# Performance work log

Hardware: AMD Instinct MI355X
Metric: run time of the kernel (lower is better)

Reference implementation:

```python
import jax, jax.numpy as jnp
import numpy as np

D = 1024      # embedding_dim
H = 16        # n_heads
HD = D // H   # head_dim
EPS = 1e-05


def layernorm(x, scale, bias):
    # torch.var default is unbiased (ddof=1) in the original module
    mean = jnp.mean(x, axis=-1, keepdims=True)
    var = jnp.var(x, axis=-1, keepdims=True, ddof=1)
    return scale * (x - mean) / jnp.sqrt(var + EPS) + bias


def gelu(x):
    return 0.5 * x * (1 + jnp.tanh(0.79788456 * (x + 0.044715 * x ** 3)))


def setup_inputs() -> dict:
    key = jax.random.key(0)
    ks = jax.random.split(key, 12)
    s = 0.02
    return {
        "x": jax.random.normal(ks[0], (2, 2048, D), dtype=jnp.float32),
        "Wq": jax.random.normal(ks[1], (D, D), dtype=jnp.float32) * s,
        "Wk": jax.random.normal(ks[2], (D, D), dtype=jnp.float32) * s,
        "Wv": jax.random.normal(ks[3], (D, D), dtype=jnp.float32) * s,
        "Wo": jax.random.normal(ks[4], (D, D), dtype=jnp.float32) * s,
        "bo": jnp.zeros((D,), dtype=jnp.float32),
        "W1": jax.random.normal(ks[5], (D, 4 * D), dtype=jnp.float32) * s,
        "b1": jnp.zeros((4 * D,), dtype=jnp.float32),
        "W2": jax.random.normal(ks[6], (4 * D, D), dtype=jnp.float32) * s,
        "b2": jnp.zeros((D,), dtype=jnp.float32),
        "ln1_scale": jnp.ones((D,), dtype=jnp.float32),
        "ln1_bias": jnp.zeros((D,), dtype=jnp.float32),
        "ln2_scale": jnp.ones((D,), dtype=jnp.float32),
        "ln2_bias": jnp.zeros((D,), dtype=jnp.float32),
    }


def reference(x, Wq, Wk, Wv, Wo, bo, W1, b1, W2, b2,
              ln1_scale, ln1_bias, ln2_scale, ln2_bias):
    B, S, _ = x.shape
    # --- attention sub-block (pre-LN) ---
    h = layernorm(x, ln1_scale, ln1_bias)
    q = (h @ Wq).reshape(B, S, H, HD).transpose(0, 2, 1, 3)  # [B,H,S,HD]
    k = (h @ Wk).reshape(B, S, H, HD).transpose(0, 2, 1, 3)
    v = (h @ Wv).reshape(B, S, H, HD).transpose(0, 2, 1, 3)
    scores = jnp.einsum("bhqd,bhkd->bhqk", q, k)             # [B,H,S,S]
    causal = jnp.tril(jnp.ones((S, S), dtype=bool))
    scores = jnp.where(causal, scores, -jnp.inf)
    attn = jax.nn.softmax(scores / jnp.sqrt(jnp.float32(HD)), axis=-1)
    ctx = jnp.einsum("bhqk,bhkd->bhqd", attn, v)
    ctx = ctx.transpose(0, 2, 1, 3).reshape(B, S, H * HD)
    x = x + (ctx @ Wo + bo)
    # --- FFN sub-block (pre-LN) ---
    h = layernorm(x, ln2_scale, ln2_bias)
    x = x + (gelu(h @ W1 + b1) @ W2 + b2)
    return x
```

## Files before the change

### kernel.cpp

```cpp
#include <hip/hip_runtime.h>
#include <hip/hip_bf16.h>
#include <cstdint>

#define D_DIM 1024
#define S_DIM 2048
#define B_DIM 2
#define NROWS 4096
#define H_DIM 16
#define LOG2E 1.4426950408889634f
#define QSCALE (0.125f * LOG2E)

typedef __bf16 bf16x8 __attribute__((ext_vector_type(8)));
typedef float f32x4 __attribute__((ext_vector_type(4)));
typedef unsigned short u16x8 __attribute__((ext_vector_type(8)));

#define MFMA16(a, b, c) __builtin_amdgcn_mfma_f32_16x16x32_bf16(a, b, c, 0, 0, 0)
#define SBAR __builtin_amdgcn_sched_barrier(0)
#define WBAR __builtin_amdgcn_s_barrier()
#define LGKM0 { asm volatile("s_waitcnt lgkmcnt(0)" ::: "memory"); SBAR; }
#define VM6 { asm volatile("s_waitcnt vmcnt(6)" ::: "memory"); SBAR; }
#define VM0 { asm volatile("s_waitcnt vmcnt(0)" ::: "memory"); SBAR; }

__device__ __forceinline__ void async_cp16(const void* g, void* lds) {
  __builtin_amdgcn_global_load_lds(
      (const __attribute__((address_space(1))) void*)(uintptr_t)g,
      (__attribute__((address_space(3))) void*)(uint32_t)(uintptr_t)lds, 16, 0, 0);
}

__device__ __forceinline__ unsigned short f2bf(float f) {
  __hip_bfloat16 h = __float2bfloat16(f);
  return __builtin_bit_cast(unsigned short, h);
}

__device__ __forceinline__ float bf2f(unsigned short u) {
  return __builtin_bit_cast(float, (unsigned int)u << 16);
}

__device__ __forceinline__ float gelu_fast(float v) {
  float u = v * v;
  float w = v * fmaf(u, 0.044715f, 1.f);
  float e = exp2f(w * -2.3022161f);
  return v * __builtin_amdgcn_rcpf(1.f + e);
}

struct TcArgs {
  const float* src[6];
  __hip_bfloat16* dst[6];
  int K[6];
  int N[6];
  int start[6];
};

__global__ __launch_bounds__(256) void transpose_cast6_kernel(TcArgs a) {
  __shared__ float tile[32][33];
  int bid = blockIdx.x, mi = 0;
#pragma unroll
  for (int i = 1; i < 6; i++)
    if (bid >= a.start[i]) mi = i;
  const float* W = a.src[mi];
  __hip_bfloat16* Wt = a.dst[mi];
  int K = a.K[mi], N = a.N[mi];
  int rel = bid - a.start[mi];
  int tilesx = N >> 5;
  int shift = (N == 4096) ? 7 : 5;
  int n0 = (rel & (tilesx - 1)) * 32, k0 = (rel >> shift) * 32;
  int tx = threadIdx.x, ty = threadIdx.y;
#pragma unroll
  for (int i = 0; i < 32; i += 8)
    tile[ty + i][tx] = W[(size_t)(k0 + ty + i) * N + n0 + tx];
  __syncthreads();
#pragma unroll
  for (int i = 0; i < 32; i += 8)
    Wt[(size_t)(n0 + ty + i) * K + k0 + tx] = __float2bfloat16(tile[tx][ty + i]);
}

__global__ __launch_bounds__(256) void ln_kernel(
    const float* __restrict__ x, const float* __restrict__ sc,
    const float* __restrict__ bi, __hip_bfloat16* __restrict__ out) {
  int row = blockIdx.x, t = threadIdx.x;
  float4 v = ((const float4*)(x + (size_t)row * D_DIM))[t];
  float s = v.x + v.y + v.z + v.w;
  float ss = v.x * v.x + v.y * v.y + v.z * v.z + v.w * v.w;
#pragma unroll
  for (int off = 32; off > 0; off >>= 1) {
    s += __shfl_xor(s, off);
    ss += __shfl_xor(ss, off);
  }
  __shared__ float red[8];
  int wid = t >> 6;
  if ((t & 63) == 0) { red[wid] = s; red[4 + wid] = ss; }
  __syncthreads();
  s = red[0] + red[1] + red[2] + red[3];
  ss = red[4] + red[5] + red[6] + red[7];
  float mean = s * (1.f / 1024.f);
  float var = (ss - 1024.f * mean * mean) * (1.f / 1023.f);
  float inv = rsqrtf(var + 1e-5f);
  float4 scv = ((const float4*)sc)[t];
  float4 biv = ((const float4*)bi)[t];
  ushort4 o;
  o.x = f2bf(scv.x * (v.x - mean) * inv + biv.x);
  o.y = f2bf(scv.y * (v.y - mean) * inv + biv.y);
  o.z = f2bf(scv.z * (v.z - mean) * inv + biv.z);
  o.w = f2bf(scv.w * (v.w - mean) * inv + biv.w);
  ((ushort4*)(out + (size_t)row * D_DIM))[t] = o;
}

template <int EPI>
__global__ __launch_bounds__(512) void gemm256_kernel(
    const __hip_bfloat16* __restrict__ A, const __hip_bfloat16* __restrict__ Bt,
    void* __restrict__ Cout, const float* __restrict__ bias,
    __hip_bfloat16* __restrict__ qb, __hip_bfloat16* __restrict__ kb,
    unsigned short* __restrict__ vt, int strideA, int strideB) {
  __shared__ char lds[131072];
  const int t = threadIdx.x;
  const int lane = t & 63, wid = t >> 6;
  const int ql = lane & 15, g = lane >> 4;
  const int wr = wid >> 2, wc = wid & 3;
  const int m0 = blockIdx.x * 256, n0 = blockIdx.y * 256;
  const int koff = blockIdx.z * 1024;
  const int sw = (ql & 7) << 4;

  const int srow = t >> 3;
  const int scol = ((t & 7) << 4) ^ ((srow & 7) << 4);
  const __hip_bfloat16* aBase = A + (size_t)(m0 + srow) * strideA + koff + (scol >> 1);
  const __hip_bfloat16* bBase = Bt + (size_t)(n0 + srow) * strideB + koff + (scol >> 1);
  const uint32_t ldsT = (uint32_t)(t * 16);

  auto stgA = [&](int kt, int half) {
    char* dst = lds + ((kt & 1) * 2 + half) * 16384 + ldsT;
    const __hip_bfloat16* src = aBase + (size_t)(half * 128) * strideA + kt * 64;
    async_cp16(src, dst);
    async_cp16(src + (size_t)64 * strideA, dst + 8192);
  };
  auto stgB = [&](int kt, int half) {
    char* dst = lds + 65536 + ((kt & 1) * 2 + half) * 16384 + ldsT;
    const __hip_bfloat16* src = bBase + (size_t)(half * 128) * strideB + kt * 64;
    async_cp16(src, dst);
    async_cp16(src + (size_t)64 * strideB, dst + 8192);
  };

  bf16x8 aR[4][2], bR[2][2][2];
  f32x4 acc[8][4] = {};

  auto ldA = [&](int slot, int mh) {
    const char* base = lds + (slot * 2 + wr) * 16384;
#pragma unroll
    for (int mi = 0; mi < 4; mi++)
#pragma unroll
      for (int kk = 0; kk < 2; kk++)
        aR[mi][kk] = *(const bf16x8*)(base + (mh * 64 + mi * 16 + ql) * 128 +
                                      ((kk * 64 + g * 16) ^ sw));
  };
  auto ldB = [&](int slot, int nh) {
    const char* base = lds + 65536 + (slot * 2 + (wc >> 1)) * 16384;
#pragma unroll
    for (int ni = 0; ni < 2; ni++)
#pragma unroll
      for (int kk = 0; kk < 2; kk++)
        bR[nh][ni][kk] = *(const bf16x8*)(base + ((wc & 1) * 64 + nh * 32 + ni * 16 + ql) * 128 +
                                          ((kk * 64 + g * 16) ^ sw));
  };
  auto mma = [&](int mh, int nh) {
    __builtin_amdgcn_s_setprio(1);
#pragma unroll
    for (int mi = 0; mi < 4; mi++)
#pragma unroll
      for (int ni = 0; ni < 2; ni++) {
        f32x4 c = acc[mh * 4 + mi][nh * 2 + ni];
        c = MFMA16(aR[mi][0], bR[nh][ni][0], c);
        c = MFMA16(aR[mi][1], bR[nh][ni][1], c);
        acc[mh * 4 + mi][nh * 2 + ni] = c;
      }
    __builtin_amdgcn_s_setprio(0);
  };

  stgB(0, 0); stgA(0, 0); stgB(0, 1); stgA(0, 1);
  stgB(1, 0); stgB(1, 1); stgA(1, 0);
  VM6; WBAR;

#pragma unroll 1
  for (int i = 0; i < 7; i++) {
    const int k2 = 2 * i;
    ldA(0, 0); ldB(0, 0); stgA(k2 + 1, 1); SBAR; WBAR; LGKM0; mma(0, 0); WBAR;
    ldB(0, 1); stgB(k2 + 2, 0); SBAR; WBAR; LGKM0; mma(0, 1); WBAR;
    ldA(0, 1); stgB(k2 + 2, 1); SBAR; WBAR; LGKM0; mma(1, 1); WBAR;
    stgA(k2 + 2, 0); SBAR; WBAR; LGKM0; mma(1, 0); VM6; WBAR;
    ldA(1, 0); ldB(1, 0); stgA(k2 + 2, 1); SBAR; WBAR; LGKM0; mma(0, 0); WBAR;
    ldB(1, 1); stgB(k2 + 3, 0); SBAR; WBAR; LGKM0; mma(0, 1); WBAR;
    ldA(1, 1); stgB(k2 + 3, 1); SBAR; WBAR; LGKM0; mma(1, 1); WBAR;
    stgA(k2 + 3, 0); SBAR; WBAR; LGKM0; mma(1, 0); VM6; WBAR;
  }
  ldA(0, 0); ldB(0, 0); stgA(15, 1); SBAR; WBAR; LGKM0; mma(0, 0); WBAR;
  ldB(0, 1); SBAR; WBAR; LGKM0; mma(0, 1); WBAR;
  ldA(0, 1); SBAR; WBAR; LGKM0; mma(1, 1); WBAR;
  SBAR; WBAR; LGKM0; mma(1, 0); VM0; WBAR;
  ldA(1, 0); ldB(1, 0); SBAR; WBAR; LGKM0; mma(0, 0); WBAR;
  ldB(1, 1); SBAR; WBAR; LGKM0; mma(0, 1); WBAR;
  ldA(1, 1); SBAR; WBAR; LGKM0; mma(1, 1); WBAR;
  mma(1, 0);

  const int rb = m0 + wr * 128 + (g << 2);
  const int cb = wc * 64 + ql;
  if (EPI == 0) {
    const int seg = n0 >> 10;
    if (seg < 2) {
      __hip_bfloat16* Ob = seg == 0 ? qb : kb;
      const float sc = seg == 0 ? QSCALE : 1.f;
#pragma unroll
      for (int mb = 0; mb < 8; mb++)
#pragma unroll
        for (int nb = 0; nb < 4; nb++) {
          int col = (n0 & 1023) + cb + nb * 16;
#pragma unroll
          for (int rr = 0; rr < 4; rr++)
            Ob[(size_t)(rb + mb * 16 + rr) * 1024 + col] =
                __float2bfloat16(acc[mb][nb][rr] * sc);
        }
    } else {
#pragma unroll
      for (int mb = 0; mb < 8; mb++)
#pragma unroll
        for (int nb = 0; nb < 4; nb++) {
          int csub = (n0 & 1023) + cb + nb * 16;
          int h = csub >> 6, dh = csub & 63;
          int row0 = rb + mb * 16;
          int bb = row0 >> 11, s0 = row0 & 2047;
          ushort4 pk;
          pk.x = f2bf(acc[mb][nb][0]);
          pk.y = f2bf(acc[mb][nb][1]);
          pk.z = f2bf(acc[mb][nb][2]);
          pk.w = f2bf(acc[mb][nb][3]);
          *(ushort4*)(vt + (((size_t)(bb * 16 + h) * 64 + dh) << 11) + s0) = pk;
        }
    }
  } else if (EPI == 1) {
#pragma unroll
    for (int mb = 0; mb < 8; mb++)
#pragma unroll
      for (int nb = 0; nb < 4; nb++) {
        int col = n0 + cb + nb * 16;
        float bv = bias[col];
#pragma unroll
        for (int rr = 0; rr < 4; rr++)
          ((__hip_bfloat16*)Cout)[(size_t)(rb + mb * 16 + rr) * 4096 + col] =
              __float2bfloat16(gelu_fast(acc[mb][nb][rr] + bv));
      }
  } else {
    unsigned short* Cp = (unsigned short*)Cout + (size_t)blockIdx.z * NROWS * 1024;
#pragma unroll
    for (int mb = 0; mb < 8; mb++)
#pragma unroll
      for (int nb = 0; nb < 4; nb++) {
        int col = n0 + cb + nb * 16;
#pragma unroll
        for (int rr = 0; rr < 4; rr++)
          Cp[(size_t)(rb + mb * 16 + rr) * 1024 + col] = f2bf(acc[mb][nb][rr]);
      }
  }
}

template <int BN, int EPI>
__global__ __launch_bounds__(256) void gemm_bt_kernel(
    const __hip_bfloat16* __restrict__ A, const __hip_bfloat16* __restrict__ Bt,
    void* __restrict__ Cout, const float* __restrict__ bias,
    const float* __restrict__ resid, int M, int N, int K, int kchunk) {
  constexpr int NBF = BN / 32;
  __shared__ __hip_bfloat16 As[2][128 * 32];
  __shared__ __hip_bfloat16 Bs[2][BN * 32];
  const int t = threadIdx.x;
  const int lane = t & 63, wid = t >> 6;
  const int ql = lane & 15, g = lane >> 4;
  const int m0 = blockIdx.x * 128, n0 = blockIdx.y * BN;
  const int kz = blockIdx.z;
  const int wm = (wid >> 1) * 64, wn = (wid & 1) * (BN / 2);
  f32x4 acc[4][NBF] = {};
  const int sr = t >> 2, sc8 = (t & 3) * 8;
  const __hip_bfloat16* ag = A + (size_t)(m0 + sr) * K + sc8 + (size_t)kz * kchunk;
  const __hip_bfloat16* bg = Bt + (size_t)(n0 + sr) * K + sc8 + (size_t)kz * kchunk;

  auto stage = [&](int buf, int k0) {
    async_cp16(ag + k0, (char*)&As[buf][0] + wid * 1024);
    async_cp16(ag + (size_t)64 * K + k0, (char*)&As[buf][0] + 4096 + wid * 1024);
    async_cp16(bg + k0, (char*)&Bs[buf][0] + wid * 1024);
    if constexpr (BN == 128)
      async_cp16(bg + (size_t)64 * K + k0, (char*)&Bs[buf][0] + 4096 + wid * 1024);
  };
  auto compute = [&](int buf) {
    bf16x8 af[4], bfr[NBF];
#pragma unroll
    for (int mb = 0; mb < 4; mb++)
      af[mb] = *(const bf16x8*)(&As[buf][(wm + mb * 16 + ql) * 32 + g * 8]);
#pragma unroll
    for (int nb = 0; nb < NBF; nb++)
      bfr[nb] = *(const bf16x8*)(&Bs[buf][(wn + nb * 16 + ql) * 32 + g * 8]);
#pragma unroll
    for (int mb = 0; mb < 4; mb++)
#pragma unroll
      for (int nb = 0; nb < NBF; nb++)
        acc[mb][nb] = MFMA16(af[mb], bfr[nb], acc[mb][nb]);
  };

  stage(0, 0);
  __syncthreads();
  const int nsteps = kchunk >> 5;
  int cur = 0;
  for (int s = 0; s < nsteps - 1; ++s) {
    stage(cur ^ 1, (s + 1) * 32);
    compute(cur);
    __syncthreads();
    cur ^= 1;
  }
  compute(cur);

  const int rb = m0 + wm + (g << 2);
  const int cb = n0 + wn + ql;
#pragma unroll
  for (int mb = 0; mb < 4; mb++) {
#pragma unroll
    for (int nb = 0; nb < NBF; nb++) {
      int col = cb + nb * 16;
#pragma unroll
      for (int r = 0; r < 4; r++) {
        int row = rb + mb * 16 + r;
        float v = acc[mb][nb][r];
        if (EPI == 1) {
          ((float*)Cout)[(size_t)row * N + col] =
              v + bias[col] + resid[(size_t)row * N + col];
        }
      }
    }
  }
}

__global__ __launch_bounds__(256) void ffn2_reduce_kernel(
    const unsigned short* __restrict__ parts, const float* __restrict__ bias,
    const float* __restrict__ resid, float* __restrict__ out) {
  const size_t i = ((size_t)blockIdx.x * 256 + threadIdx.x) * 8;
  const int col = (int)(i & 1023);
  float a[8];
  float4 r0 = *(const float4*)(resid + i);
  float4 r1 = *(const float4*)(resid + i + 4);
  float4 b0 = *(const float4*)(bias + col);
  float4 b1 = *(const float4*)(bias + col + 4);
  a[0] = r0.x + b0.x; a[1] = r0.y + b0.y; a[2] = r0.z + b0.z; a[3] = r0.w + b0.w;
  a[4] = r1.x + b1.x; a[5] = r1.y + b1.y; a[6] = r1.z + b1.z; a[7] = r1.w + b1.w;
#pragma unroll
  for (int c = 0; c < 4; c++) {
    u16x8 p = *(const u16x8*)(parts + (size_t)c * ((size_t)NROWS * 1024) + i);
#pragma unroll
    for (int j = 0; j < 8; j++) a[j] += bf2f(p[j]);
  }
  float4 o0 = {a[0], a[1], a[2], a[3]};
  float4 o1 = {a[4], a[5], a[6], a[7]};
  *(float4*)(out + i) = o0;
  *(float4*)(out + i + 4) = o1;
}

__global__ __launch_bounds__(256) void attn_kernel(
    const __hip_bfloat16* __restrict__ Q, const __hip_bfloat16* __restrict__ Kb,
    const __hip_bfloat16* __restrict__ Vt, __hip_bfloat16* __restrict__ ctx) {
  __shared__ unsigned short Ks[2][64 * 64];
  __shared__ unsigned short Vs[2][64 * 64];
  __shared__ alignas(16) unsigned short Ps[4][16 * 64];
  const int t = threadIdx.x;
  const int lane = t & 63, wid = t >> 6;
  const int ql = lane & 15, g = lane >> 4;
  const int bid = blockIdx.x;
  const int r4 = bid >> 8, k8 = (bid >> 5) & 7, bh = bid & 31;
  const int qt = (r4 == 0) ? 31 - k8 : (r4 == 1) ? 16 + k8 : (r4 == 2) ? 15 - k8 : k8;
  const int b = bh >> 4, hh = bh & 15;
  const int wq0 = qt * 64 + wid * 16;
  const __hip_bfloat16* qp = Q + (size_t)b * S_DIM * D_DIM + hh * 64;
  const __hip_bfloat16* kp = Kb + (size_t)b * S_DIM * D_DIM + hh * 64;
  const __hip_bfloat16* vp = Vt + (size_t)bh * 64 * S_DIM;
  const int kvend = qt * 64 + 64;
  const int swz = (ql & 7) << 4;
  const f32x4 z4 = {0.f, 0.f, 0.f, 0.f};

  auto stageKV = [&](int buf, int kv0) {
    const int sub = lane >> 3, c = lane & 7;
#pragma unroll
    for (int i = 0; i < 2; i++) {
      const int row = wid * 16 + i * 8 + sub;
      const int cs = (c ^ (row & 7)) * 8;
      async_cp16(kp + (size_t)(kv0 + row) * D_DIM + cs,
                 (char*)&Ks[buf][0] + (wid * 16 + i * 8) * 128);
      async_cp16(vp + (size_t)row * S_DIM + kv0 + cs,
                 (char*)&Vs[buf][0] + (wid * 16 + i * 8) * 128);
    }
  };

  bf16x8 qf[2];
#pragma unroll
  for (int hf = 0; hf < 2; hf++)
    qf[hf] = *(const bf16x8*)(qp + (size_t)(wq0 + ql) * D_DIM + hf * 32 + g * 8);

  float m = -3.0e38f, lsum = 0.f;
  f32x4 acc[4] = {};
  unsigned short* Pw = Ps[wid];

  stageKV(0, 0);
  __syncthreads();
  int cur = 0;
  for (int kv0 = 0; kv0 < kvend; kv0 += 64) {
    if (kv0 + 64 < kvend) stageKV(cur ^ 1, kv0 + 64);

    if (kv0 <= wq0 + 15) {
      const char* Kt = (const char*)&Ks[cur][0];
      f32x4 st[4];
#pragma unroll
      for (int ks = 0; ks < 4; ks++) {
        bf16x8 k0 = *(const bf16x8*)(Kt + (ks * 16 + ql) * 128 + ((g * 16) ^ swz));
        bf16x8 k1 = *(const bf16x8*)(Kt + (ks * 16 + ql) * 128 + (((4 + g) * 16) ^ swz));
        st[ks] = MFMA16(k1, qf[1], MFMA16(k0, qf[0], z4));
      }
      if (kv0 + 63 > wq0) {
#pragma unroll
        for (int ks = 0; ks < 4; ks++)
#pragma unroll
          for (int r = 0; r < 4; r++)
            if (kv0 + ks * 16 + 4 * g + r > wq0 + ql) st[ks][r] = -3.0e38f;
      }
      float tm = -3.0e38f;
#pragma unroll
      for (int ks = 0; ks < 4; ks++)
#pragma unroll
        for (int r = 0; r < 4; r++) tm = fmaxf(tm, st[ks][r]);
      tm = fmaxf(tm, __shfl_xor(tm, 16));
      tm = fmaxf(tm, __shfl_xor(tm, 32));
      if (!__all(tm <= m + 8.f)) {
        const float mn = fmaxf(m, tm);
        const float alpha = exp2f(m - mn);
        lsum *= alpha;
#pragma unroll
        for (int db = 0; db < 4; db++) acc[db] *= alpha;
        m = mn;
      }
      float psum = 0.f;
#pragma unroll
      for (int ks = 0; ks < 4; ks++) {
        float p0 = exp2f(st[ks][0] - m), p1 = exp2f(st[ks][1] - m);
        float p2 = exp2f(st[ks][2] - m), p3 = exp2f(st[ks][3] - m);
        psum += (p0 + p1) + (p2 + p3);
        ushort4 pk;
        pk.x = f2bf(p0); pk.y = f2bf(p1); pk.z = f2bf(p2); pk.w = f2bf(p3);
        *(ushort4*)((char*)Pw + ql * 128 + ((ks * 32 + 8 * g) ^ swz)) = pk;
      }
      psum += __shfl_xor(psum, 16);
      psum += __shfl_xor(psum, 32);
      lsum += psum;

      const char* Vtl = (const char*)&Vs[cur][0];
#pragma unroll
      for (int ksl = 0; ksl < 2; ksl++) {
        bf16x8 pb = *(const bf16x8*)((const char*)Pw + ql * 128 + ((ksl * 64 + 16 * g) ^ swz));
#pragma unroll
        for (int db = 0; db < 4; db++) {
          bf16x8 va = *(const bf16x8*)(Vtl + (db * 16 + ql) * 128 + (((ksl * 4 + g) * 16) ^ swz));
          acc[db] = MFMA16(va, pb, acc[db]);
        }
      }
    }
    __syncthreads();
    cur ^= 1;
  }

  const float inv = 1.f / lsum;
  unsigned short* cp = (unsigned short*)ctx + (size_t)(b * S_DIM + wq0 + ql) * D_DIM + hh * 64;
#pragma unroll
  for (int db = 0; db < 4; db++)
#pragma unroll
    for (int i = 0; i < 2; i++) {
      unsigned int lo = f2bf(acc[db][2 * i] * inv);
      unsigned int hi = f2bf(acc[db][2 * i + 1] * inv);
      *(unsigned int*)(cp + db * 16 + 4 * g + 2 * i) = lo | (hi << 16);
    }
}

extern "C" void kernel_launch(void* const* d_in, const int* in_sizes, int n_in,
                              void* d_out, int out_size, void* d_ws, size_t ws_size,
                              hipStream_t stream) {
  const float* x = (const float*)d_in[0];
  const float* Wq = (const float*)d_in[1];
  const float* Wk = (const float*)d_in[2];
  const float* Wv = (const float*)d_in[3];
  const float* Wo = (const float*)d_in[4];
  const float* bo = (const float*)d_in[5];
  const float* W1 = (const float*)d_in[6];
  const float* b1 = (const float*)d_in[7];
  const float* W2 = (const float*)d_in[8];
  const float* b2 = (const float*)d_in[9];
  const float* ln1s = (const float*)d_in[10];
  const float* ln1b = (const float*)d_in[11];
  const float* ln2s = (const float*)d_in[12];
  const float* ln2b = (const float*)d_in[13];
  float* out = (float*)d_out;

  char* p = (char*)d_ws;
  auto take = [&](size_t n) { char* r = p; p += (n + 255) & ~(size_t)255; return r; };
  __hip_bfloat16* Wqt = (__hip_bfloat16*)take((size_t)1024 * 1024 * 2);
  __hip_bfloat16* Wkt = (__hip_bfloat16*)take((size_t)1024 * 1024 * 2);
  __hip_bfloat16* Wvt = (__hip_bfloat16*)take((size_t)1024 * 1024 * 2);
  __hip_bfloat16* Wot = (__hip_bfloat16*)take((size_t)1024 * 1024 * 2);
  __hip_bfloat16* W1t = (__hip_bfloat16*)take((size_t)4096 * 1024 * 2);
  __hip_bfloat16* W2t = (__hip_bfloat16*)take((size_t)4096 * 1024 * 2);
  __hip_bfloat16* hbuf = (__hip_bfloat16*)take((size_t)NROWS * 1024 * 2);
  __hip_bfloat16* qbuf = (__hip_bfloat16*)take((size_t)NROWS * 1024 * 2);
  __hip_bfloat16* kbuf = (__hip_bfloat16*)take((size_t)NROWS * 1024 * 2);
  __hip_bfloat16* vtbuf = (__hip_bfloat16*)take((size_t)NROWS * 1024 * 2);
  __hip_bfloat16* ctxbuf = (__hip_bfloat16*)take((size_t)NROWS * 1024 * 2);
  float* x1buf = (float*)take((size_t)NROWS * 1024 * 4);
  __hip_bfloat16* h2buf = (__hip_bfloat16*)take((size_t)NROWS * 1024 * 2);
  __hip_bfloat16* gbuf = (__hip_bfloat16*)take((size_t)NROWS * 4096 * 2);
  unsigned short* parts = (unsigned short*)hbuf;

  TcArgs ta;
  ta.src[0] = Wq;  ta.dst[0] = Wqt;  ta.K[0] = 1024; ta.N[0] = 1024; ta.start[0] = 0;
  ta.src[1] = Wk;  ta.dst[1] = Wkt;  ta.K[1] = 1024; ta.N[1] = 1024; ta.start[1] = 1024;
  ta.src[2] = Wv;  ta.dst[2] = Wvt;  ta.K[2] = 1024; ta.N[2] = 1024; ta.start[2] = 2048;
  ta.src[3] = Wo;  ta.dst[3] = Wot;  ta.K[3] = 1024; ta.N[3] = 1024; ta.start[3] = 3072;
  ta.src[4] = W1;  ta.dst[4] = W1t;  ta.K[4] = 1024; ta.N[4] = 4096; ta.start[4] = 4096;
  ta.src[5] = W2;  ta.dst[5] = W2t;  ta.K[5] = 4096; ta.N[5] = 1024; ta.start[5] = 8192;
  transpose_cast6_kernel<<<12288, dim3(32, 8), 0, stream>>>(ta);

  ln_kernel<<<NROWS, 256, 0, stream>>>(x, ln1s, ln1b, hbuf);

  gemm256_kernel<0><<<dim3(16, 12), 512, 0, stream>>>(
      hbuf, Wqt, nullptr, nullptr, qbuf, kbuf, (unsigned short*)vtbuf, 1024, 1024);

  attn_kernel<<<1024, 256, 0, stream>>>(qbuf, kbuf, vtbuf, ctxbuf);

  gemm_bt_kernel<64, 1><<<dim3(32, 16, 1), 256, 0, stream>>>(
      ctxbuf, Wot, x1buf, bo, x, NROWS, 1024, 1024, 1024);

  ln_kernel<<<NROWS, 256, 0, stream>>>(x1buf, ln2s, ln2b, h2buf);

  gemm256_kernel<1><<<dim3(16, 16), 512, 0, stream>>>(
      h2buf, W1t, gbuf, b1, nullptr, nullptr, nullptr, 1024, 1024);

  gemm256_kernel<2><<<dim3(16, 4, 4), 512, 0, stream>>>(
      gbuf, W2t, parts, nullptr, nullptr, nullptr, nullptr, 4096, 4096);

  ffn2_reduce_kernel<<<2048, 256, 0, stream>>>(parts, b2, x1buf, out);
}
```

Baseline: 205.8 us.

## Restructure 256x256 GEMM pipeline with half-tile waits and interleaved warp tile mapping

Changes the warp-to-tile mapping so each warp's A rows and B columns come from both staged LDS halves (interleaved 64-row/32-col slices) instead of one half. The main loop is rescheduled to wait for individual staged halves with fine-grained vmcnt counts. It also drops the explicit lgkmcnt(0) waits and full sched barriers, using a partial sched_barrier mask that lets the compiler place LDS waits. The epilogue is rewritten to match the new accumulator layout. The goal is to overlap global-to-LDS copies with MFMA more tightly and cut barrier stalls, at the risk of subtle ordering bugs in the vmcnt accounting.

```diff
diff --git a/kernel.cpp b/kernel.cpp
--- a/kernel.cpp
+++ b/kernel.cpp
@@ -15,11 +15,9 @@
 typedef unsigned short u16x8 __attribute__((ext_vector_type(8)));
 
 #define MFMA16(a, b, c) __builtin_amdgcn_mfma_f32_16x16x32_bf16(a, b, c, 0, 0, 0)
-#define SBAR __builtin_amdgcn_sched_barrier(0)
+#define SBM __builtin_amdgcn_sched_barrier(0x0F)
 #define WBAR __builtin_amdgcn_s_barrier()
-#define LGKM0 { asm volatile("s_waitcnt lgkmcnt(0)" ::: "memory"); SBAR; }
-#define VM6 { asm volatile("s_waitcnt vmcnt(6)" ::: "memory"); SBAR; }
-#define VM0 { asm volatile("s_waitcnt vmcnt(0)" ::: "memory"); SBAR; }
+#define VMW(n) asm volatile("s_waitcnt vmcnt(" #n ")" ::: "memory")
 
 __device__ __forceinline__ void async_cp16(const void* g, void* lds) {
   __builtin_amdgcn_global_load_lds(
@@ -126,39 +124,37 @@
   const __hip_bfloat16* bBase = Bt + (size_t)(n0 + srow) * strideB + koff + (scol >> 1);
   const uint32_t ldsT = (uint32_t)(t * 16);
 
-  auto stgA = [&](int kt, int half) {
-    char* dst = lds + ((kt & 1) * 2 + half) * 16384 + ldsT;
-    const __hip_bfloat16* src = aBase + (size_t)(half * 128) * strideA + kt * 64;
+  auto stgA = [&](int kt, int h) {
+    char* dst = lds + (((kt & 1) * 2 + h) * 16384) + ldsT;
+    const __hip_bfloat16* src = aBase + (size_t)(h * 128) * strideA + kt * 64;
     async_cp16(src, dst);
     async_cp16(src + (size_t)64 * strideA, dst + 8192);
   };
-  auto stgB = [&](int kt, int half) {
-    char* dst = lds + 65536 + ((kt & 1) * 2 + half) * 16384 + ldsT;
-    const __hip_bfloat16* src = bBase + (size_t)(half * 128) * strideB + kt * 64;
+  auto stgB = [&](int kt, int h) {
+    char* dst = lds + 65536 + (((kt & 1) * 2 + h) * 16384) + ldsT;
+    const __hip_bfloat16* src = bBase + (size_t)(h * 128) * strideB + kt * 64;
     async_cp16(src, dst);
     async_cp16(src + (size_t)64 * strideB, dst + 8192);
   };
 
   bf16x8 aR[4][2], bR[2][2][2];
-  f32x4 acc[8][4] = {};
+  f32x4 acc[2][4][2][2] = {};
 
   auto ldA = [&](int slot, int mh) {
-    const char* base = lds + (slot * 2 + wr) * 16384;
+    const char* base = lds + ((slot * 2 + mh) * 16384) + (wr * 64 + ql) * 128;
 #pragma unroll
     for (int mi = 0; mi < 4; mi++)
 #pragma unroll
       for (int kk = 0; kk < 2; kk++)
-        aR[mi][kk] = *(const bf16x8*)(base + (mh * 64 + mi * 16 + ql) * 128 +
-                                      ((kk * 64 + g * 16) ^ sw));
+        aR[mi][kk] = *(const bf16x8*)(base + mi * 2048 + ((kk * 64 + g * 16) ^ sw));
   };
   auto ldB = [&](int slot, int nh) {
-    const char* base = lds + 65536 + (slot * 2 + (wc >> 1)) * 16384;
+    const char* base = lds + 65536 + ((slot * 2 + nh) * 16384) + (wc * 32 + ql) * 128;
 #pragma unroll
     for (int ni = 0; ni < 2; ni++)
 #pragma unroll
       for (int kk = 0; kk < 2; kk++)
-        bR[nh][ni][kk] = *(const bf16x8*)(base + ((wc & 1) * 64 + nh * 32 + ni * 16 + ql) * 128 +
-                                          ((kk * 64 + g * 16) ^ sw));
+        bR[nh][ni][kk] = *(const bf16x8*)(base + ni * 2048 + ((kk * 64 + g * 16) ^ sw));
   };
   auto mma = [&](int mh, int nh) {
     __builtin_amdgcn_s_setprio(1);
@@ -166,96 +162,82 @@
     for (int mi = 0; mi < 4; mi++)
 #pragma unroll
       for (int ni = 0; ni < 2; ni++) {
-        f32x4 c = acc[mh * 4 + mi][nh * 2 + ni];
+        f32x4 c = acc[mh][mi][nh][ni];
         c = MFMA16(aR[mi][0], bR[nh][ni][0], c);
         c = MFMA16(aR[mi][1], bR[nh][ni][1], c);
-        acc[mh * 4 + mi][nh * 2 + ni] = c;
+        acc[mh][mi][nh][ni] = c;
       }
     __builtin_amdgcn_s_setprio(0);
   };
 
-  stgB(0, 0); stgA(0, 0); stgB(0, 1); stgA(0, 1);
-  stgB(1, 0); stgB(1, 1); stgA(1, 0);
-  VM6; WBAR;
+  stgB(0, 0); stgA(0, 0); stgB(0, 1); stgA(0, 1); stgB(1, 0);
+  VMW(6); SBM; WBAR;
 
 #pragma unroll 1
   for (int i = 0; i < 7; i++) {
-    const int k2 = 2 * i;
-    ldA(0, 0); ldB(0, 0); stgA(k2 + 1, 1); SBAR; WBAR; LGKM0; mma(0, 0); WBAR;
-    ldB(0, 1); stgB(k2 + 2, 0); SBAR; WBAR; LGKM0; mma(0, 1); WBAR;
-    ldA(0, 1); stgB(k2 + 2, 1); SBAR; WBAR; LGKM0; mma(1, 1); WBAR;
-    stgA(k2 + 2, 0); SBAR; WBAR; LGKM0; mma(1, 0); VM6; WBAR;
-    ldA(1, 0); ldB(1, 0); stgA(k2 + 2, 1); SBAR; WBAR; LGKM0; mma(0, 0); WBAR;
-    ldB(1, 1); stgB(k2 + 3, 0); SBAR; WBAR; LGKM0; mma(0, 1); WBAR;
-    ldA(1, 1); stgB(k2 + 3, 1); SBAR; WBAR; LGKM0; mma(1, 1); WBAR;
-    stgA(k2 + 3, 0); SBAR; WBAR; LGKM0; mma(1, 0); VM6; WBAR;
-  }
-  ldA(0, 0); ldB(0, 0); stgA(15, 1); SBAR; WBAR; LGKM0; mma(0, 0); WBAR;
-  ldB(0, 1); SBAR; WBAR; LGKM0; mma(0, 1); WBAR;
-  ldA(0, 1); SBAR; WBAR; LGKM0; mma(1, 1); WBAR;
-  SBAR; WBAR; LGKM0; mma(1, 0); VM0; WBAR;
-  ldA(1, 0); ldB(1, 0); SBAR; WBAR; LGKM0; mma(0, 0); WBAR;
-  ldB(1, 1); SBAR; WBAR; LGKM0; mma(0, 1); WBAR;
-  ldA(1, 1); SBAR; WBAR; LGKM0; mma(1, 1); WBAR;
-  mma(1, 0);
-
-  const int rb = m0 + wr * 128 + (g << 2);
-  const int cb = wc * 64 + ql;
-  if (EPI == 0) {
-    const int seg = n0 >> 10;
-    if (seg < 2) {
-      __hip_bfloat16* Ob = seg == 0 ? qb : kb;
-      const float sc = seg == 0 ? QSCALE : 1.f;
-#pragma unroll
-      for (int mb = 0; mb < 8; mb++)
-#pragma unroll
-        for (int nb = 0; nb < 4; nb++) {
-          int col = (n0 & 1023) + cb + nb * 16;
-#pragma unroll
-          for (int rr = 0; rr < 4; rr++)
-            Ob[(size_t)(rb + mb * 16 + rr) * 1024 + col] =
-                __float2bfloat16(acc[mb][nb][rr] * sc);
+    const int o = 2 * i + 1, e2 = 2 * i + 2, o2 = 2 * i + 3;
+    ldA(0, 0); ldB(0, 0); stgA(o, 0);  VMW(6); SBM; WBAR; mma(0, 0);
+    ldB(0, 1);            stgB(o, 1);  VMW(6); SBM; WBAR; mma(0, 1);
+    ldA(0, 1);            stgA(o, 1);          SBM; WBAR; mma(1, 1);
+                          stgB(e2, 0); VMW(6); SBM; WBAR; mma(1, 0);
+    ldA(1, 0); ldB(1, 0); stgA(e2, 0); VMW(6); SBM; WBAR; mma(0, 0);
+    ldB(1, 1);            stgB(e2, 1); VMW(6); SBM; WBAR; mma(0, 1);
+    ldA(1, 1);            stgA(e2, 1);         SBM; WBAR; mma(1, 1);
+                          stgB(o2, 0); VMW(6); SBM; WBAR; mma(1, 0);
+  }
+  ldA(0, 0); ldB(0, 0); stgA(15, 0); VMW(6); SBM; WBAR; mma(0, 0);
+  ldB(0, 1);            stgB(15, 1); VMW(6); SBM; WBAR; mma(0, 1);
+  ldA(0, 1);            stgA(15, 1);         SBM; WBAR; mma(1, 1);
+                                     VMW(4); SBM; WBAR; mma(1, 0);
+  ldA(1, 0); ldB(1, 0);              VMW(2); SBM; WBAR; mma(0, 0);
+  ldB(1, 1);                         VMW(0); SBM; WBAR; mma(0, 1);
+  ldA(1, 1);                                 SBM; WBAR; mma(1, 1);
+                                                        mma(1, 0);
+
+#pragma unroll
+  for (int mh = 0; mh < 2; mh++) {
+#pragma unroll
+    for (int mi = 0; mi < 4; mi++) {
+      const int row0 = m0 + mh * 128 + wr * 64 + mi * 16 + g * 4;
+#pragma unroll
+      for (int nh = 0; nh < 2; nh++) {
+#pragma unroll
+        for (int ni = 0; ni < 2; ni++) {
+          const int colt = nh * 128 + wc * 32 + ni * 16 + ql;
+          const f32x4 c = acc[mh][mi][nh][ni];
+          if (EPI == 0) {
+            const int seg = n0 >> 10;
+            const int c1k = (n0 & 1023) + colt;
+            if (seg < 2) {
+              __hip_bfloat16* Ob = seg == 0 ? qb : kb;
+              const float sc = seg == 0 ? QSCALE : 1.f;
+#pragma unroll
+              for (int rr = 0; rr < 4; rr++)
+                Ob[(size_t)(row0 + rr) * 1024 + c1k] = __float2bfloat16(c[rr] * sc);
+            } else {
+              const int h = c1k >> 6, dh = c1k & 63;
+              const int bb = row0 >> 11, s0 = row0 & 2047;
+              ushort4 pk;
+              pk.x = f2bf(c[0]); pk.y = f2bf(c[1]); pk.z = f2bf(c[2]); pk.w = f2bf(c[3]);
+              *(ushort4*)(vt + (((size_t)(bb * 16 + h) * 64 + dh) << 11) + s0) = pk;
+            }
+          } else if (EPI == 1) {
+            const int col = n0 + colt;
+            const float bv = bias[col];
+#pragma unroll
+            for (int rr = 0; rr < 4; rr++)
+              ((__hip_bfloat16*)Cout)[(size_t)(row0 + rr) * 4096 + col] =
+                  __float2bfloat16(gelu_fast(c[rr] + bv));
+          } else {
+            unsigned short* Cp = (unsigned short*)Cout + (size_t)blockIdx.z * NROWS * 1024;
+            const int col = n0 + colt;
+#pragma unroll
+            for (int rr = 0; rr < 4; rr++)
+              Cp[(size_t)(row0 + rr) * 1024 + col] = f2bf(c[rr]);
+          }
         }
-    } else {
-#pragma unroll
-      for (int mb = 0; mb < 8; mb++)
-#pragma unroll
-        for (int nb = 0; nb < 4; nb++) {
-          int csub = (n0 & 1023) + cb + nb * 16;
-          int h = csub >> 6, dh = csub & 63;
-          int row0 = rb + mb * 16;
-          int bb = row0 >> 11, s0 = row0 & 2047;
-          ushort4 pk;
-          pk.x = f2bf(acc[mb][nb][0]);
-          pk.y = f2bf(acc[mb][nb][1]);
-          pk.z = f2bf(acc[mb][nb][2]);
-          pk.w = f2bf(acc[mb][nb][3]);
-          *(ushort4*)(vt + (((size_t)(bb * 16 + h) * 64 + dh) << 11) + s0) = pk;
-        }
+      }
     }
-  } else if (EPI == 1) {
-#pragma unroll
-    for (int mb = 0; mb < 8; mb++)
-#pragma unroll
-      for (int nb = 0; nb < 4; nb++) {
-        int col = n0 + cb + nb * 16;
-        float bv = bias[col];
-#pragma unroll
-        for (int rr = 0; rr < 4; rr++)
-          ((__hip_bfloat16*)Cout)[(size_t)(rb + mb * 16 + rr) * 4096 + col] =
-              __float2bfloat16(gelu_fast(acc[mb][nb][rr] + bv));
-      }
-  } else {
-    unsigned short* Cp = (unsigned short*)Cout + (size_t)blockIdx.z * NROWS * 1024;
-#pragma unroll
-    for (int mb = 0; mb < 8; mb++)
-#pragma unroll
-      for (int nb = 0; nb < 4; nb++) {
-        int col = n0 + cb + nb * 16;
-#pragma unroll
-        for (int rr = 0; rr < 4; rr++)
-          Cp[(size_t)(rb + mb * 16 + rr) * 1024 + col] = f2bf(acc[mb][nb][rr]);
-      }
   }
 }
 
```

Result: no change. 209.7 us (+1.9%).
